# Kernel optimization log

Hardware: AMD Instinct MI355X
Metric: run time of the kernel (lower is better)

## Reference

```python
import jax, jax.numpy as jnp
import numpy as np

S, C1, C2, N = 4096, 2048, 2048, 1024


def setup_inputs() -> dict:
    key = jax.random.key(0)
    k1, k2, k3, k4 = jax.random.split(key, 4)
    # child log-likelihoods (samples, child_nodes); modest scale so exp() stays finite,
    # matching the (numerically naive) torch forward which exps without max-subtraction.
    ll1 = jax.random.normal(k1, (S, C1), dtype=jnp.float32)
    ll2 = jax.random.normal(k2, (S, C2), dtype=jnp.float32)
    # log edge weights, one tensor per child layer: (nodes, child_nodes)
    w1 = jax.random.normal(k3, (N, C1), dtype=jnp.float32)
    w2 = jax.random.normal(k4, (N, C2), dtype=jnp.float32)
    return {"ll1": ll1, "ll2": ll2, "w1": w1, "w2": w2}


def reference(ll1, ll2, w1, w2):
    # Per child layer: sum_c exp(ll[s,c] + w[n,c]) == exp(ll) @ exp(w).T  -> (S, N)
    # (same math as unsqueeze/repeat/exp/sum in the torch code, without the (S,C,N) blowup)
    result = jnp.exp(ll1) @ jnp.exp(w1).T + jnp.exp(ll2) @ jnp.exp(w2).T  # (S, N)
    # per-node log normalization constant over concatenated weights
    log_z = jax.nn.logsumexp(jnp.concatenate([w1, w2], axis=1), axis=1)  # (N,)
    return jnp.log(result) - log_z[None, :]
```

## Files before the change

kernel.cpp:

```cpp
#include <hip/hip_runtime.h>

#define S_DIM 4096
#define C_DIM 2048
#define N_DIM 1024
#define K_DIM 4096

#define BM 128
#define BN 128
#define BK 32
#define NT (K_DIM / BK)
#define TILE_BYTES 16384
#define NBUF 8

typedef __attribute__((ext_vector_type(8))) short bf16x8;
typedef __attribute__((ext_vector_type(8))) unsigned short u16x8;
typedef __attribute__((ext_vector_type(4))) float f32x4;

__device__ static inline unsigned short f2bf(float f) {
    unsigned int u = __float_as_uint(f);
    u += 0x7FFFu + ((u >> 16) & 1u);
    return (unsigned short)(u >> 16);
}

__global__ void prepass_kernel(const float* __restrict__ ll1,
                               const float* __restrict__ ll2,
                               const float* __restrict__ w1,
                               const float* __restrict__ w2,
                               unsigned short* __restrict__ A,
                               unsigned short* __restrict__ B,
                               float* __restrict__ lz) {
    __shared__ float red[4];
    __shared__ float red2[4];
    const int tid = threadIdx.x;

    if (blockIdx.x < N_DIM) {
        const int n = blockIdx.x;
        const int lane = tid & 63, wv = tid >> 6;
        const float* r1 = w1 + ((size_t)n << 11);
        const float* r2 = w2 + ((size_t)n << 11);
        float4 v0 = *reinterpret_cast<const float4*>(r1 + tid * 8);
        float4 v1 = *reinterpret_cast<const float4*>(r1 + tid * 8 + 4);
        float4 u0 = *reinterpret_cast<const float4*>(r2 + tid * 8);
        float4 u1 = *reinterpret_cast<const float4*>(r2 + tid * 8 + 4);

        float mx = fmaxf(fmaxf(fmaxf(v0.x, v0.y), fmaxf(v0.z, v0.w)),
                         fmaxf(fmaxf(v1.x, v1.y), fmaxf(v1.z, v1.w)));
        mx = fmaxf(mx, fmaxf(fmaxf(fmaxf(u0.x, u0.y), fmaxf(u0.z, u0.w)),
                              fmaxf(fmaxf(u1.x, u1.y), fmaxf(u1.z, u1.w))));
        #pragma unroll
        for (int off = 32; off > 0; off >>= 1) mx = fmaxf(mx, __shfl_xor(mx, off));
        if (lane == 0) red[wv] = mx;
        __syncthreads();
        mx = fmaxf(fmaxf(red[0], red[1]), fmaxf(red[2], red[3]));

        float s = __expf(v0.x - mx) + __expf(v0.y - mx) + __expf(v0.z - mx) + __expf(v0.w - mx)
                + __expf(v1.x - mx) + __expf(v1.y - mx) + __expf(v1.z - mx) + __expf(v1.w - mx)
                + __expf(u0.x - mx) + __expf(u0.y - mx) + __expf(u0.z - mx) + __expf(u0.w - mx)
                + __expf(u1.x - mx) + __expf(u1.y - mx) + __expf(u1.z - mx) + __expf(u1.w - mx);
        #pragma unroll
        for (int off = 32; off > 0; off >>= 1) s += __shfl_xor(s, off);
        if (lane == 0) red2[wv] = s;
        __syncthreads();
        if (tid == 0)
            lz[n] = mx + __logf(red2[0] + red2[1] + red2[2] + red2[3]);

        unsigned short* brow = B + ((size_t)n << 12);
        u16x8 o;
        o[0] = f2bf(__expf(v0.x)); o[1] = f2bf(__expf(v0.y));
        o[2] = f2bf(__expf(v0.z)); o[3] = f2bf(__expf(v0.w));
        o[4] = f2bf(__expf(v1.x)); o[5] = f2bf(__expf(v1.y));
        o[6] = f2bf(__expf(v1.z)); o[7] = f2bf(__expf(v1.w));
        *reinterpret_cast<u16x8*>(brow + tid * 8) = o;
        o[0] = f2bf(__expf(u0.x)); o[1] = f2bf(__expf(u0.y));
        o[2] = f2bf(__expf(u0.z)); o[3] = f2bf(__expf(u0.w));
        o[4] = f2bf(__expf(u1.x)); o[5] = f2bf(__expf(u1.y));
        o[6] = f2bf(__expf(u1.z)); o[7] = f2bf(__expf(u1.w));
        *reinterpret_cast<u16x8*>(brow + C_DIM + tid * 8) = o;
        return;
    }

    const int bid = blockIdx.x - N_DIM;
    const int total8 = S_DIM * C_DIM / 8;
    const int stride = 2048 * 256;
    for (int i = bid * 256 + tid; i < total8; i += stride) {
        int e = i << 3;
        int r = e >> 11;
        int c = e & 2047;
        size_t dst = ((size_t)r << 12) + c;
        float4 v0 = *reinterpret_cast<const float4*>(ll1 + e);
        float4 v1 = *reinterpret_cast<const float4*>(ll1 + e + 4);
        u16x8 o;
        o[0] = f2bf(__expf(v0.x)); o[1] = f2bf(__expf(v0.y));
        o[2] = f2bf(__expf(v0.z)); o[3] = f2bf(__expf(v0.w));
        o[4] = f2bf(__expf(v1.x)); o[5] = f2bf(__expf(v1.y));
        o[6] = f2bf(__expf(v1.z)); o[7] = f2bf(__expf(v1.w));
        *reinterpret_cast<u16x8*>(A + dst) = o;
        float4 u0 = *reinterpret_cast<const float4*>(ll2 + e);
        float4 u1 = *reinterpret_cast<const float4*>(ll2 + e + 4);
        o[0] = f2bf(__expf(u0.x)); o[1] = f2bf(__expf(u0.y));
        o[2] = f2bf(__expf(u0.z)); o[3] = f2bf(__expf(u0.w));
        o[4] = f2bf(__expf(u1.x)); o[5] = f2bf(__expf(u1.y));
        o[6] = f2bf(__expf(u1.z)); o[7] = f2bf(__expf(u1.w));
        *reinterpret_cast<u16x8*>(A + dst + C_DIM) = o;
    }
}

typedef const unsigned int __attribute__((address_space(1)))* gas_ptr;
typedef unsigned int __attribute__((address_space(3)))* las_ptr;

__global__ __launch_bounds__(512, 2) void gemm_log_kernel(
        const unsigned short* __restrict__ A,
        const unsigned short* __restrict__ B,
        const float* __restrict__ lz,
        float* __restrict__ out) {
    __shared__ __align__(16) char lds[NBUF * TILE_BYTES];
    const int tid  = threadIdx.x;
    const int l    = tid & 63;
    const int w    = tid >> 6;
    const int bn = blockIdx.x & 7;
    const int bm = blockIdx.x >> 3;

#define GLOAD(p_, o_) __builtin_amdgcn_global_load_lds((gas_ptr)(const void*)(p_), \
        (las_ptr)(void*)(lds + (o_)), 16, 0, 0)

    if (w >= 4) {
        const int pw = w - 4;
        const int kg = (l & 3) ^ ((l >> 3) & 3);
        const unsigned short* src[4];
        int dst[4];
        #pragma unroll
        for (int i = 0; i < 4; ++i) {
            const int ri  = pw * 4 + i;
            const int row = ri * 16 + (l >> 2);
            src[i] = (ri < 8)
                ? A + (size_t)(bm * BM + row) * K_DIM + kg * 8
                : B + (size_t)(bn * BN + row - 128) * K_DIM + kg * 8;
            dst[i] = row * 64 + (l & 3) * 16;
        }
#define STAGE(T, BUFI) { const int _ko = (T) * BK; const int _bo = (BUFI) * TILE_BYTES; \
        GLOAD(src[0] + _ko, _bo + dst[0]); GLOAD(src[1] + _ko, _bo + dst[1]);           \
        GLOAD(src[2] + _ko, _bo + dst[2]); GLOAD(src[3] + _ko, _bo + dst[3]); }
#define PBODY(T, BUFI, WAITN) {                                                         \
        asm volatile("s_waitcnt vmcnt(" #WAITN ")" ::: "memory");                       \
        __builtin_amdgcn_s_barrier();                                                   \
        STAGE((T) + 8, BUFI); }

        STAGE(0, 0); STAGE(1, 1); STAGE(2, 2); STAGE(3, 3);
        STAGE(4, 4); STAGE(5, 5); STAGE(6, 6); STAGE(7, 7);
        asm volatile("s_waitcnt vmcnt(28)" ::: "memory");
        __builtin_amdgcn_s_barrier();
        for (int t8 = 0; t8 < NT - 8; t8 += 8) {
            PBODY(t8 + 0, 0, 24); PBODY(t8 + 1, 1, 24);
            PBODY(t8 + 2, 2, 24); PBODY(t8 + 3, 3, 24);
            PBODY(t8 + 4, 4, 24); PBODY(t8 + 5, 5, 24);
            PBODY(t8 + 6, 6, 24); PBODY(t8 + 7, 7, 24);
        }
        asm volatile("s_waitcnt vmcnt(24)" ::: "memory"); __builtin_amdgcn_s_barrier();
        asm volatile("s_waitcnt vmcnt(20)" ::: "memory"); __builtin_amdgcn_s_barrier();
        asm volatile("s_waitcnt vmcnt(16)" ::: "memory"); __builtin_amdgcn_s_barrier();
        asm volatile("s_waitcnt vmcnt(12)" ::: "memory"); __builtin_amdgcn_s_barrier();
        asm volatile("s_waitcnt vmcnt(8)"  ::: "memory"); __builtin_amdgcn_s_barrier();
        asm volatile("s_waitcnt vmcnt(4)"  ::: "memory"); __builtin_amdgcn_s_barrier();
        asm volatile("s_waitcnt vmcnt(0)"  ::: "memory"); __builtin_amdgcn_s_barrier();
#undef PBODY
#undef STAGE
    } else {
        const int wr = w >> 1, wc = w & 1;
        const int lcol = l & 15, lk = l >> 4;
        const int swz = (lk ^ ((lcol >> 1) & 3)) << 4;
        int aoff[4], boff[4];
        #pragma unroll
        for (int m = 0; m < 4; ++m) aoff[m] = (wr * 64 + m * 16 + lcol) * 64 + swz;
        #pragma unroll
        for (int n = 0; n < 4; ++n) boff[n] = 8192 + (wc * 64 + n * 16 + lcol) * 64 + swz;

        f32x4 acc[4][4] = {};
        bf16x8 a0[4], b0[4], a1[4], b1[4];

#define READF(RBUF, AR, BR) { const char* _rb = lds + (RBUF) * TILE_BYTES;              \
        _Pragma("unroll") for (int m = 0; m < 4; ++m)                                   \
            AR[m] = *reinterpret_cast<const bf16x8*>(_rb + aoff[m]);                    \
        _Pragma("unroll") for (int n = 0; n < 4; ++n)                                   \
            BR[n] = *reinterpret_cast<const bf16x8*>(_rb + boff[n]); }
#define MFMAS(AMM, BMM) {                                                               \
        __builtin_amdgcn_s_setprio(1);                                                  \
        _Pragma("unroll") for (int m = 0; m < 4; ++m)                                   \
            _Pragma("unroll") for (int n = 0; n < 4; ++n)                               \
                acc[m][n] = __builtin_amdgcn_mfma_f32_16x16x32_bf16(AMM[m], BMM[n],     \
                                                                    acc[m][n], 0, 0, 0);\
        __builtin_amdgcn_s_setprio(0); }
#define CBODY(T, RB, AR, BR, AMM, BMM) {                                                \
        __builtin_amdgcn_s_barrier();                                                   \
        READF(RB, AR, BR);                                                              \
        MFMAS(AMM, BMM); }

        __builtin_amdgcn_s_barrier();
        READF(0, a0, b0);
        for (int t8 = 0; t8 < NT - 8; t8 += 8) {
            CBODY(t8 + 0, 1, a1, b1, a0, b0);
            CBODY(t8 + 1, 2, a0, b0, a1, b1);
            CBODY(t8 + 2, 3, a1, b1, a0, b0);
            CBODY(t8 + 3, 4, a0, b0, a1, b1);
            CBODY(t8 + 4, 5, a1, b1, a0, b0);
            CBODY(t8 + 5, 6, a0, b0, a1, b1);
            CBODY(t8 + 6, 7, a1, b1, a0, b0);
            CBODY(t8 + 7, 0, a0, b0, a1, b1);
        }
        CBODY(120, 1, a1, b1, a0, b0);
        CBODY(121, 2, a0, b0, a1, b1);
        CBODY(122, 3, a1, b1, a0, b0);
        CBODY(123, 4, a0, b0, a1, b1);
        CBODY(124, 5, a1, b1, a0, b0);
        CBODY(125, 6, a0, b0, a1, b1);
        CBODY(126, 7, a1, b1, a0, b0);
        MFMAS(a1, b1);
#undef CBODY
#undef MFMAS
#undef READF

        const int col_base = bn * BN + wc * 64;
        float lzv[4];
        #pragma unroll
        for (int n = 0; n < 4; ++n) lzv[n] = lz[col_base + n * 16 + lcol];
        #pragma unroll
        for (int m = 0; m < 4; ++m) {
            const int row0 = bm * BM + wr * 64 + m * 16 + lk * 4;
            #pragma unroll
            for (int n = 0; n < 4; ++n) {
                const int col = col_base + n * 16 + lcol;
                #pragma unroll
                for (int j = 0; j < 4; ++j)
                    out[(size_t)(row0 + j) * N_DIM + col] = __logf(acc[m][n][j]) - lzv[n];
            }
        }
    }
#undef GLOAD
}

__global__ void naive_kernel(const float* __restrict__ ll1, const float* __restrict__ ll2,
                             const float* __restrict__ w1, const float* __restrict__ w2,
                             float* __restrict__ out) {
    int idx = blockIdx.x * blockDim.x + threadIdx.x;
    if (idx >= S_DIM * N_DIM) return;
    int s = idx >> 10, n = idx & (N_DIM - 1);
    const float* a1 = ll1 + (size_t)s * C_DIM;
    const float* a2 = ll2 + (size_t)s * C_DIM;
    const float* b1 = w1 + (size_t)n * C_DIM;
    const float* b2 = w2 + (size_t)n * C_DIM;
    float mx = -3.0e38f;
    for (int c = 0; c < C_DIM; ++c) mx = fmaxf(mx, b1[c]);
    for (int c = 0; c < C_DIM; ++c) mx = fmaxf(mx, b2[c]);
    float zs = 0.f, acc = 0.f;
    for (int c = 0; c < C_DIM; ++c) { zs += __expf(b1[c] - mx); acc += __expf(a1[c] + b1[c]); }
    for (int c = 0; c < C_DIM; ++c) { zs += __expf(b2[c] - mx); acc += __expf(a2[c] + b2[c]); }
    out[idx] = __logf(acc) - (mx + __logf(zs));
}

extern "C" void kernel_launch(void* const* d_in, const int* in_sizes, int n_in,
                              void* d_out, int out_size, void* d_ws, size_t ws_size,
                              hipStream_t stream) {
    const float* ll1 = (const float*)d_in[0];
    const float* ll2 = (const float*)d_in[1];
    const float* w1  = (const float*)d_in[2];
    const float* w2  = (const float*)d_in[3];
    float* out = (float*)d_out;

    const size_t a_elems = (size_t)S_DIM * K_DIM;
    const size_t b_elems = (size_t)N_DIM * K_DIM;
    const size_t need = (a_elems + b_elems) * sizeof(unsigned short) + N_DIM * sizeof(float);
    if (ws_size < need) {
        naive_kernel<<<(S_DIM * N_DIM + 255) / 256, 256, 0, stream>>>(ll1, ll2, w1, w2, out);
        return;
    }
    unsigned short* Aws = (unsigned short*)d_ws;
    unsigned short* Bws = Aws + a_elems;
    float* lzws = (float*)(Bws + b_elems);

    prepass_kernel<<<N_DIM + 2048, 256, 0, stream>>>(ll1, ll2, w1, w2, Aws, Bws, lzws);
    gemm_log_kernel<<<(S_DIM / BM) * (N_DIM / BN), 512, 0, stream>>>(Aws, Bws, lzws, out);
}
```

Baseline: 67.94 us.

## Add split-K GEMM with larger 256x128 tiles plus a separate log-reduce kernel

Adds a new GEMM path that splits K into two halves and uses 256x128 output tiles with 6 LDS buffers and one block per CU. Each half writes a bf16 partial product to workspace, and a separate elementwise kernel sums the two halves, takes the log and subtracts lz. The intent is more work per block and a better grid fill on the GPU (256 blocks). In exchange it adds an extra kernel launch and a 16 MB round-trip of partials through memory. Storing partials in bf16 also loses precision before the log.

```diff
diff --git a/kernel.cpp b/kernel.cpp
--- a/kernel.cpp
+++ b/kernel.cpp
@@ -5,9 +5,17 @@
 #define N_DIM 1024
 #define K_DIM 4096
 
+#define BM3 256
+#define BN3 128
+#define KS3 2
+#define KSL3 (K_DIM / KS3)
+#define BK 32
+#define NT3 (KSL3 / BK)
+#define TILE3 24576
+#define NBUF3 6
+
 #define BM 128
 #define BN 128
-#define BK 32
 #define NT (K_DIM / BK)
 #define TILE_BYTES 16384
 #define NBUF 8
@@ -20,6 +28,9 @@
     unsigned int u = __float_as_uint(f);
     u += 0x7FFFu + ((u >> 16) & 1u);
     return (unsigned short)(u >> 16);
+}
+__device__ static inline float bf2f(unsigned short h) {
+    return __uint_as_float((unsigned int)h << 16);
 }
 
 __global__ void prepass_kernel(const float* __restrict__ ll1,
@@ -108,6 +119,140 @@
 typedef const unsigned int __attribute__((address_space(1)))* gas_ptr;
 typedef unsigned int __attribute__((address_space(3)))* las_ptr;
 
+__global__ __launch_bounds__(512, 1) void gemm_ks2_kernel(
+        const unsigned short* __restrict__ A,
+        const unsigned short* __restrict__ B,
+        unsigned short* __restrict__ P) {
+    __shared__ __align__(16) char lds[NBUF3 * TILE3];
+    const int tid  = threadIdx.x;
+    const int l    = tid & 63;
+    const int w    = tid >> 6;
+    const int wg   = blockIdx.x;
+    const int bn   = wg & 7;
+    const int bm   = (wg >> 3) & 15;
+    const int ks   = wg >> 7;
+
+#define GLOAD(p_, o_) __builtin_amdgcn_global_load_lds((gas_ptr)(const void*)(p_), \
+        (las_ptr)(void*)(lds + (o_)), 16, 0, 0)
+
+    if (w >= 4) {
+        const int pw = w - 4;
+        const int kg = (l & 3) ^ ((l >> 3) & 3);
+        const unsigned short* src[6];
+        int dst[6];
+        #pragma unroll
+        for (int i = 0; i < 6; ++i) {
+            const int ri  = pw * 6 + i;
+            const int row = ri * 16 + (l >> 2);
+            src[i] = (ri < 16)
+                ? A + (size_t)(bm * BM3 + row) * K_DIM + ks * KSL3 + kg * 8
+                : B + (size_t)(bn * BN3 + row - 256) * K_DIM + ks * KSL3 + kg * 8;
+            dst[i] = row * 64 + (l & 3) * 16;
+        }
+#define STAGE(T, BUFI) { const int _ko = (T) * BK; const int _bo = (BUFI) * TILE3;  \
+        GLOAD(src[0] + _ko, _bo + dst[0]); GLOAD(src[1] + _ko, _bo + dst[1]);       \
+        GLOAD(src[2] + _ko, _bo + dst[2]); GLOAD(src[3] + _ko, _bo + dst[3]);       \
+        GLOAD(src[4] + _ko, _bo + dst[4]); GLOAD(src[5] + _ko, _bo + dst[5]); }
+#define PBODY(T, BUFI) {                                                            \
+        asm volatile("s_waitcnt vmcnt(18)" ::: "memory");                           \
+        __builtin_amdgcn_s_barrier();                                               \
+        STAGE((T) + 5, BUFI); }
+
+        STAGE(0, 0); STAGE(1, 1); STAGE(2, 2); STAGE(3, 3); STAGE(4, 4);
+        asm volatile("s_waitcnt vmcnt(24)" ::: "memory");
+        __builtin_amdgcn_s_barrier();
+        for (int t6 = 0; t6 < 54; t6 += 6) {
+            PBODY(t6 + 0, 5); PBODY(t6 + 1, 0); PBODY(t6 + 2, 1);
+            PBODY(t6 + 3, 2); PBODY(t6 + 4, 3); PBODY(t6 + 5, 4);
+        }
+        PBODY(54, 5); PBODY(55, 0); PBODY(56, 1);
+        PBODY(57, 2); PBODY(58, 3);
+        asm volatile("s_waitcnt vmcnt(18)" ::: "memory"); __builtin_amdgcn_s_barrier();
+        asm volatile("s_waitcnt vmcnt(12)" ::: "memory"); __builtin_amdgcn_s_barrier();
+        asm volatile("s_waitcnt vmcnt(6)"  ::: "memory"); __builtin_amdgcn_s_barrier();
+        asm volatile("s_waitcnt vmcnt(0)"  ::: "memory"); __builtin_amdgcn_s_barrier();
+#undef PBODY
+#undef STAGE
+    } else {
+        const int lcol = l & 15, lk = l >> 4;
+        const int swz = (lk ^ ((lcol >> 1) & 3)) << 4;
+        const int abase = (w * 64 + lcol) * 64 + swz;
+        const int bbase = 16384 + lcol * 64 + swz;
+
+        f32x4 acc[4][8] = {};
+        bf16x8 a0[4], b0[8], a1[4], b1[8];
+
+#define READF(RBUF, AR, BR) { const char* _rb = lds + (RBUF) * TILE3;               \
+        _Pragma("unroll") for (int m = 0; m < 4; ++m)                               \
+            AR[m] = *reinterpret_cast<const bf16x8*>(_rb + abase + m * 1024);       \
+        _Pragma("unroll") for (int n = 0; n < 8; ++n)                               \
+            BR[n] = *reinterpret_cast<const bf16x8*>(_rb + bbase + n * 1024); }
+#define MFMAS(AMM, BMM) {                                                           \
+        __builtin_amdgcn_s_setprio(1);                                              \
+        _Pragma("unroll") for (int m = 0; m < 4; ++m)                               \
+            _Pragma("unroll") for (int n = 0; n < 8; ++n)                           \
+                acc[m][n] = __builtin_amdgcn_mfma_f32_16x16x32_bf16(AMM[m], BMM[n], \
+                                                                    acc[m][n], 0, 0, 0); \
+        __builtin_amdgcn_s_setprio(0); }
+#define CBODY(RB, AR, BR, AMM, BMM) {                                               \
+        __builtin_amdgcn_s_barrier();                                               \
+        READF(RB, AR, BR);                                                          \
+        MFMAS(AMM, BMM); }
+
+        __builtin_amdgcn_s_barrier();
+        READF(0, a0, b0);
+        for (int t6 = 0; t6 < 60; t6 += 6) {
+            CBODY(1, a1, b1, a0, b0); CBODY(2, a0, b0, a1, b1);
+            CBODY(3, a1, b1, a0, b0); CBODY(4, a0, b0, a1, b1);
+            CBODY(5, a1, b1, a0, b0); CBODY(0, a0, b0, a1, b1);
+        }
+        CBODY(1, a1, b1, a0, b0);
+        CBODY(2, a0, b0, a1, b1);
+        CBODY(3, a1, b1, a0, b0);
+        MFMAS(a1, b1);
+#undef CBODY
+#undef MFMAS
+#undef READF
+
+        unsigned short* Pk = P + (size_t)ks * ((size_t)S_DIM * N_DIM);
+        const int col_base = bn * BN3;
+        #pragma unroll
+        for (int m = 0; m < 4; ++m) {
+            const int row0 = bm * BM3 + w * 64 + m * 16 + lk * 4;
+            #pragma unroll
+            for (int n = 0; n < 8; ++n) {
+                const int col = col_base + n * 16 + lcol;
+                #pragma unroll
+                for (int j = 0; j < 4; ++j)
+                    Pk[(size_t)(row0 + j) * N_DIM + col] = f2bf(acc[m][n][j]);
+            }
+        }
+    }
+#undef GLOAD
+}
+
+__global__ void reduce_kernel(const unsigned short* __restrict__ P,
+                              const float* __restrict__ lz,
+                              float* __restrict__ out) {
+    const size_t SN = (size_t)S_DIM * N_DIM;
+    int i = blockIdx.x * blockDim.x + threadIdx.x;
+    size_t e = (size_t)i * 8;
+    int n = (int)(e & (N_DIM - 1));
+    u16x8 p0 = *reinterpret_cast<const u16x8*>(P + e);
+    u16x8 p1 = *reinterpret_cast<const u16x8*>(P + SN + e);
+    float4 lz0 = *reinterpret_cast<const float4*>(lz + n);
+    float4 lz1 = *reinterpret_cast<const float4*>(lz + n + 4);
+    float lzv[8] = {lz0.x, lz0.y, lz0.z, lz0.w, lz1.x, lz1.y, lz1.z, lz1.w};
+    float o[8];
+    #pragma unroll
+    for (int j = 0; j < 8; ++j) {
+        float s = bf2f((unsigned short)p0[j]) + bf2f((unsigned short)p1[j]);
+        o[j] = __logf(s) - lzv[j];
+    }
+    *reinterpret_cast<float4*>(out + e)     = make_float4(o[0], o[1], o[2], o[3]);
+    *reinterpret_cast<float4*>(out + e + 4) = make_float4(o[4], o[5], o[6], o[7]);
+}
+
 __global__ __launch_bounds__(512, 2) void gemm_log_kernel(
         const unsigned short* __restrict__ A,
         const unsigned short* __restrict__ B,
@@ -267,8 +412,10 @@
 
     const size_t a_elems = (size_t)S_DIM * K_DIM;
     const size_t b_elems = (size_t)N_DIM * K_DIM;
-    const size_t need = (a_elems + b_elems) * sizeof(unsigned short) + N_DIM * sizeof(float);
-    if (ws_size < need) {
+    const size_t sn      = (size_t)S_DIM * N_DIM;
+    const size_t need1 = (a_elems + b_elems) * sizeof(unsigned short) + N_DIM * sizeof(float);
+    const size_t need2 = need1 + KS3 * sn * sizeof(unsigned short);
+    if (ws_size < need1) {
         naive_kernel<<<(S_DIM * N_DIM + 255) / 256, 256, 0, stream>>>(ll1, ll2, w1, w2, out);
         return;
     }
@@ -277,5 +424,12 @@
     float* lzws = (float*)(Bws + b_elems);
 
     prepass_kernel<<<N_DIM + 2048, 256, 0, stream>>>(ll1, ll2, w1, w2, Aws, Bws, lzws);
-    gemm_log_kernel<<<(S_DIM / BM) * (N_DIM / BN), 512, 0, stream>>>(Aws, Bws, lzws, out);
-}
+
+    if (ws_size >= need2) {
+        unsigned short* Pws = (unsigned short*)(lzws + N_DIM);
+        gemm_ks2_kernel<<<(S_DIM / BM3) * (N_DIM / BN3) * KS3, 512, 0, stream>>>(Aws, Bws, Pws);
+        reduce_kernel<<<(int)(sn / 8 / 256), 256, 0, stream>>>(Pws, lzws, out);
+    } else {
+        gemm_log_kernel<<<(S_DIM / BM) * (N_DIM / BN), 512, 0, stream>>>(Aws, Bws, lzws, out);
+    }
+}
```

Result: slower. 75.25 us (+10.8%).
